# Kernel tuning notes

Measured on AMD Instinct MI355X. Metric: run time of the kernel, lower is better.

The kernel has to match this reference:

```python
import jax, jax.numpy as jnp
import numpy as np

ALPHA = 0.2          # LeakyReLU negative slope
NEG_BIG = -9e15      # zero_vec value used before softmax masking


def setup_inputs() -> dict:
    key = jax.random.key(0)
    k1, k2, k3, k4, k5 = jax.random.split(key, 5)
    N, M, F, K = 2048, 8192, 1024, 10
    feature_matrix = jax.random.normal(k1, (N, F), dtype=jnp.float32)
    embed_matrix = jax.random.normal(k2, (M, F), dtype=jnp.float32)
    # Xavier-ish scaling for params
    weight = jax.random.normal(k3, (F, F), dtype=jnp.float32) * (1.0 / np.sqrt(F))
    a = jax.random.normal(k4, (2 * F, 1), dtype=jnp.float32) * (1.0 / np.sqrt(2 * F))
    neigh_idx = jax.random.randint(k5, (N, K), 0, M, dtype=jnp.int64)
    return {
        "feature_matrix": feature_matrix,
        "embed_matrix": embed_matrix,
        "weight": weight,
        "a": a,
        "neigh_idx": neigh_idx,
    }


def reference(feature_matrix, embed_matrix, weight, a, neigh_idx):
    # feature_matrix: [N, F] features of batch nodes
    # embed_matrix:   [M, F] features of unique sampled neighbors
    # neigh_idx:      [N, K] sampled neighbor columns (set semantics: dups collapse)
    N, F = feature_matrix.shape
    M = embed_matrix.shape[0]
    rows = jnp.arange(N)[:, None]
    mask = jnp.zeros((N, M), dtype=feature_matrix.dtype).at[rows, neigh_idx].set(1.0)

    # GAT kernel path
    hf = feature_matrix @ weight          # [N, F]
    he = embed_matrix @ weight            # [M, F]
    # e_ij = leakyrelu([h_i || h_j] . a) == leakyrelu(h_i.a1 + h_j.a2)
    a1 = a[:F, 0]
    a2 = a[F:, 0]
    e = (hf @ a1)[:, None] + (he @ a2)[None, :]          # [N, M]
    e = jnp.where(e > 0, e, ALPHA * e)                   # LeakyReLU(0.2)
    scores = jnp.where(mask > 0, e, NEG_BIG)
    attention = jax.nn.softmax(scores, axis=1)           # row softmax
    to_feats = attention @ he                            # [N, F]
    return to_feats
```

## Files before the change

### kernel.cpp

```cpp
#include <hip/hip_runtime.h>
#include <math.h>

#define ALPHA 0.2f
#define MAXK 10

typedef _Float16 half8 __attribute__((ext_vector_type(8)));
typedef _Float16 half4 __attribute__((ext_vector_type(4)));
typedef float f32x4 __attribute__((ext_vector_type(4)));

__device__ __forceinline__ void gload_lds16(const void* g, void* l) {
    __builtin_amdgcn_global_load_lds(
        (const __attribute__((address_space(1))) unsigned int*)g,
        (__attribute__((address_space(3))) unsigned int*)l, 16, 0, 0);
}

__global__ void wa_kernel(const float* __restrict__ W, const float* __restrict__ a,
                          float* __restrict__ wa, int F) {
    int wave = (int)((blockIdx.x * blockDim.x + threadIdx.x) >> 6);
    int lane = threadIdx.x & 63;
    if (wave >= F) return;
    const float4* wr = reinterpret_cast<const float4*>(W + (size_t)wave * F);
    const float4* a1 = reinterpret_cast<const float4*>(a);
    const float4* a2 = reinterpret_cast<const float4*>(a + F);
    float acc1 = 0.f, acc2 = 0.f;
    int F4 = F >> 2;
    for (int c = lane; c < F4; c += 64) {
        float4 w = wr[c];
        float4 x = a1[c];
        float4 y = a2[c];
        acc1 += w.x * x.x + w.y * x.y + w.z * x.z + w.w * x.w;
        acc2 += w.x * y.x + w.y * y.y + w.z * y.z + w.w * y.w;
    }
    #pragma unroll
    for (int off = 32; off; off >>= 1) {
        acc1 += __shfl_down(acc1, off);
        acc2 += __shfl_down(acc2, off);
    }
    if (lane == 0) { wa[wave] = acc1; wa[F + wave] = acc2; }
}

__global__ __launch_bounds__(256) void mid_kernel(
    const float* __restrict__ feat, const float* __restrict__ embed,
    const int* __restrict__ nidx, const float* __restrict__ wa,
    const float* __restrict__ W, _Float16* __restrict__ agg,
    _Float16* __restrict__ Wt, int F, int N) {
    const int tid = threadIdx.x;

    if ((int)blockIdx.x >= N) {
        __shared__ float t[32][33];
        const int tb = blockIdx.x - N;
        const int tpr = F >> 5;
        const int bx = (tb % tpr) * 32;
        const int by = (tb / tpr) * 32;
        const int x = tid & 31, y = tid >> 5;
        for (int i = y; i < 32; i += 8)
            t[i][x] = W[(size_t)(bx + i) * F + by + x];
        __syncthreads();
        for (int i = y; i < 32; i += 8)
            Wt[(size_t)(by + i) * F + bx + x] = (_Float16)t[x][i];
        return;
    }

    const int i = blockIdx.x;
    const int f = tid * 4;

    int idx[MAXK];
    bool dup[MAXK];
    #pragma unroll
    for (int k = 0; k < MAXK; k++) idx[k] = nidx[i * MAXK + k];
    #pragma unroll
    for (int k = 0; k < MAXK; k++) {
        bool d = false;
        #pragma unroll
        for (int p = 0; p < MAXK; p++)
            if (p < k) d |= (idx[p] == idx[k]);
        dup[k] = d;
    }

    float4 wa1 = *(const float4*)&wa[f];
    float4 wa2 = *(const float4*)&wa[F + f];
    float4 fv  = *(const float4*)&feat[(size_t)i * F + f];
    float a1p = fv.x * wa1.x + fv.y * wa1.y + fv.z * wa1.z + fv.w * wa1.w;

    float4 rv[MAXK];
    float a2p[MAXK];
    #pragma unroll
    for (int k = 0; k < MAXK; k++) {
        rv[k] = *(const float4*)&embed[(size_t)idx[k] * F + f];
        a2p[k] = rv[k].x * wa2.x + rv[k].y * wa2.y + rv[k].z * wa2.z + rv[k].w * wa2.w;
    }

    #pragma unroll
    for (int off = 32; off; off >>= 1) {
        a1p += __shfl_down(a1p, off);
        #pragma unroll
        for (int k = 0; k < MAXK; k++) a2p[k] += __shfl_down(a2p[k], off);
    }
    __shared__ float red[MAXK + 1][4];
    const int w = tid >> 6, l = tid & 63;
    if (l == 0) {
        red[0][w] = a1p;
        #pragma unroll
        for (int k = 0; k < MAXK; k++) red[k + 1][w] = a2p[k];
    }
    __syncthreads();

    float s1 = red[0][0] + red[0][1] + red[0][2] + red[0][3];
    float sc[MAXK];
    float m = -INFINITY;
    #pragma unroll
    for (int k = 0; k < MAXK; k++) {
        float v = s1 + red[k + 1][0] + red[k + 1][1] + red[k + 1][2] + red[k + 1][3];
        v = v > 0.f ? v : ALPHA * v;
        sc[k] = v;
        if (!dup[k]) m = fmaxf(m, v);
    }
    float sum = 0.f;
    #pragma unroll
    for (int k = 0; k < MAXK; k++) {
        sc[k] = dup[k] ? 0.f : expf(sc[k] - m);
        sum += sc[k];
    }
    float inv = 1.0f / sum;

    float4 o = make_float4(0.f, 0.f, 0.f, 0.f);
    #pragma unroll
    for (int k = 0; k < MAXK; k++) {
        float wk = sc[k] * inv;
        o.x += wk * rv[k].x;
        o.y += wk * rv[k].y;
        o.z += wk * rv[k].z;
        o.w += wk * rv[k].w;
    }
    half4 h = { (_Float16)o.x, (_Float16)o.y, (_Float16)o.z, (_Float16)o.w };
    *(half4*)&agg[(size_t)i * F + f] = h;
}

__global__ __launch_bounds__(256) void gemm_f16_kernel(
    const _Float16* __restrict__ A, const _Float16* __restrict__ Bt,
    float* __restrict__ C, int M, int N, int K) {
    __shared__ _Float16 As[2][64 * 128];
    __shared__ _Float16 Bs[2][64 * 128];
    const int tid = threadIdx.x;

    int bid = blockIdx.y * gridDim.x + blockIdx.x;
    int nwg = gridDim.x * gridDim.y;
    int cpx = nwg >> 3;
    int wg = (bid & 7) * cpx + (bid >> 3);
    const int m0 = (wg / gridDim.x) * 64;
    const int n0 = (wg % gridDim.x) * 64;

    const int l = tid & 63, wv = tid >> 6;
    const int wm = wv >> 1, wn = wv & 1;
    const int lrow = l & 15, kc = l >> 4;
    const int nt = K >> 7;

    f32x4 acc[2][2] = {};

    #define STAGE(bf, t)                                                            \
    do {                                                                            \
        int k0_ = (t) * 128;                                                        \
        _Pragma("unroll")                                                           \
        for (int j_ = 0; j_ < 4; j_++) {                                            \
            int u_ = wv * 256 + j_ * 64 + l;                                        \
            int row_ = u_ >> 4, slot_ = (u_ & 15) ^ (row_ & 7);                     \
            gload_lds16(&A[(size_t)(m0 + row_) * K + k0_ + slot_ * 8],              \
                        (void*)((char*)&As[bf][0] + u_ * 16));                      \
        }                                                                           \
        _Pragma("unroll")                                                           \
        for (int j_ = 0; j_ < 4; j_++) {                                            \
            int u_ = wv * 256 + j_ * 64 + l;                                        \
            int row_ = u_ >> 4, slot_ = (u_ & 15) ^ (row_ & 7);                     \
            gload_lds16(&Bt[(size_t)(n0 + row_) * K + k0_ + slot_ * 8],             \
                        (void*)((char*)&Bs[bf][0] + u_ * 16));                      \
        }                                                                           \
    } while (0)

    STAGE(0, 0);

    int buf = 0;
    for (int t = 0; t < nt; ++t) {
        if (t + 1 < nt) {
            STAGE(buf ^ 1, t + 1);
            asm volatile("s_waitcnt vmcnt(8)" ::: "memory");
        } else {
            asm volatile("s_waitcnt vmcnt(0)" ::: "memory");
        }
        __builtin_amdgcn_s_barrier();
        __builtin_amdgcn_sched_barrier(0);

        __builtin_amdgcn_s_setprio(1);
        #pragma unroll
        for (int ks = 0; ks < 4; ks++) {
            half8 av[2], bv[2];
            #pragma unroll
            for (int fq = 0; fq < 2; fq++) {
                int arow = wm * 32 + fq * 16 + lrow;
                int ag = (ks * 4 + kc) ^ (arow & 7);
                av[fq] = *(const half8*)((const char*)&As[buf][0] + arow * 256 + ag * 16);
                int brow = wn * 32 + fq * 16 + lrow;
                int bg = (ks * 4 + kc) ^ (brow & 7);
                bv[fq] = *(const half8*)((const char*)&Bs[buf][0] + brow * 256 + bg * 16);
            }
            #pragma unroll
            for (int fq = 0; fq < 2; fq++)
                #pragma unroll
                for (int g = 0; g < 2; g++)
                    acc[fq][g] = __builtin_amdgcn_mfma_f32_16x16x32_f16(
                        av[fq], bv[g], acc[fq][g], 0, 0, 0);
        }
        __builtin_amdgcn_s_setprio(0);

        __builtin_amdgcn_sched_barrier(0);
        __builtin_amdgcn_s_barrier();
        buf ^= 1;
    }
    #undef STAGE

    #pragma unroll
    for (int fq = 0; fq < 2; fq++)
        #pragma unroll
        for (int g = 0; g < 2; g++)
            #pragma unroll
            for (int r = 0; r < 4; r++)
                C[(size_t)(m0 + wm * 32 + fq * 16 + kc * 4 + r) * N
                  + n0 + wn * 32 + g * 16 + lrow] = acc[fq][g][r];
}

extern "C" void kernel_launch(void* const* d_in, const int* in_sizes, int n_in,
                              void* d_out, int out_size, void* d_ws, size_t ws_size,
                              hipStream_t stream) {
    const float* feat  = (const float*)d_in[0];
    const float* embed = (const float*)d_in[1];
    const float* W     = (const float*)d_in[2];
    const float* a     = (const float*)d_in[3];
    const int*   nidx  = (const int*)d_in[4];

    int F = in_sizes[3] / 2;
    int N = in_sizes[0] / F;
    int M = in_sizes[1] / F;

    float* ws = (float*)d_ws;
    float* wa = ws;
    _Float16* agg_f16 = (_Float16*)(wa + 2 * F);
    _Float16* wt_f16  = agg_f16 + (size_t)N * F;
    (void)M;

    wa_kernel<<<(F * 64 + 255) / 256, 256, 0, stream>>>(W, a, wa, F);
    {
        int tblocks = (F / 32) * (F / 32);
        mid_kernel<<<N + tblocks, 256, 0, stream>>>(feat, embed, nidx, wa, W,
                                                    agg_f16, wt_f16, F, N);
    }
    {
        dim3 grid(F / 64, N / 64);
        gemm_f16_kernel<<<grid, 256, 0, stream>>>(agg_f16, wt_f16, (float*)d_out, N, F, F);
    }
}
```

Measured before the change: 36.79 us.

## Map one wavefront per row in aggregation kernel to drop block-level reduction

The aggregation part of mid_kernel now processes four rows per 256-thread block, one row per wavefront, instead of one row per block. Each lane covers four float4 chunks of the feature dimension, so the scores are reduced entirely with xor shuffles and the shared-memory reduction plus __syncthreads is gone. In exchange, the gathered embedding rows are no longer held in registers between score and aggregation; they are reloaded from global memory (likely L2-cached) for the weighted sum. The hard-coded 4x64 chunk loop assumes F == 1024 and N divisible by 4.

```diff
diff --git a/kernel.cpp b/kernel.cpp
--- a/kernel.cpp
+++ b/kernel.cpp
@@ -12,6 +12,10 @@
     __builtin_amdgcn_global_load_lds(
         (const __attribute__((address_space(1))) unsigned int*)g,
         (__attribute__((address_space(3))) unsigned int*)l, 16, 0, 0);
+}
+
+__device__ __forceinline__ float dot4(float4 a, float4 b) {
+    return a.x * b.x + a.y * b.y + a.z * b.z + a.w * b.w;
 }
 
 __global__ void wa_kernel(const float* __restrict__ W, const float* __restrict__ a,
@@ -28,8 +32,8 @@
         float4 w = wr[c];
         float4 x = a1[c];
         float4 y = a2[c];
-        acc1 += w.x * x.x + w.y * x.y + w.z * x.z + w.w * x.w;
-        acc2 += w.x * y.x + w.y * y.y + w.z * y.z + w.w * y.w;
+        acc1 += dot4(w, x);
+        acc2 += dot4(w, y);
     }
     #pragma unroll
     for (int off = 32; off; off >>= 1) {
@@ -45,10 +49,11 @@
     const float* __restrict__ W, _Float16* __restrict__ agg,
     _Float16* __restrict__ Wt, int F, int N) {
     const int tid = threadIdx.x;
-
-    if ((int)blockIdx.x >= N) {
+    const int nAgg = N >> 2;
+
+    if ((int)blockIdx.x >= nAgg) {
         __shared__ float t[32][33];
-        const int tb = blockIdx.x - N;
+        const int tb = blockIdx.x - nAgg;
         const int tpr = F >> 5;
         const int bx = (tb % tpr) * 32;
         const int by = (tb / tpr) * 32;
@@ -61,8 +66,13 @@
         return;
     }
 
-    const int i = blockIdx.x;
-    const int f = tid * 4;
+    const int wv = tid >> 6, lane = tid & 63;
+    const int i = (blockIdx.x << 2) | wv;
+    const int F4 = F >> 2;
+
+    const float4* e4 = reinterpret_cast<const float4*>(embed);
+    const float4* f4 = reinterpret_cast<const float4*>(feat);
+    const float4* w4 = reinterpret_cast<const float4*>(wa);
 
     int idx[MAXK];
     bool dup[MAXK];
@@ -77,40 +87,39 @@
         dup[k] = d;
     }
 
-    float4 wa1 = *(const float4*)&wa[f];
-    float4 wa2 = *(const float4*)&wa[F + f];
-    float4 fv  = *(const float4*)&feat[(size_t)i * F + f];
-    float a1p = fv.x * wa1.x + fv.y * wa1.y + fv.z * wa1.z + fv.w * wa1.w;
-
-    float4 rv[MAXK];
+    float4 w2[4];
+    #pragma unroll
+    for (int j = 0; j < 4; j++) w2[j] = w4[F4 + j * 64 + lane];
+
+    float a1p = 0.f;
+    #pragma unroll
+    for (int j = 0; j < 4; j++) {
+        float4 fv = f4[(size_t)i * F4 + j * 64 + lane];
+        float4 w1 = w4[j * 64 + lane];
+        a1p += dot4(fv, w1);
+    }
     float a2p[MAXK];
     #pragma unroll
     for (int k = 0; k < MAXK; k++) {
-        rv[k] = *(const float4*)&embed[(size_t)idx[k] * F + f];
-        a2p[k] = rv[k].x * wa2.x + rv[k].y * wa2.y + rv[k].z * wa2.z + rv[k].w * wa2.w;
+        float s = 0.f;
+        #pragma unroll
+        for (int j = 0; j < 4; j++)
+            s += dot4(e4[(size_t)idx[k] * F4 + j * 64 + lane], w2[j]);
+        a2p[k] = s;
     }
 
     #pragma unroll
     for (int off = 32; off; off >>= 1) {
-        a1p += __shfl_down(a1p, off);
-        #pragma unroll
-        for (int k = 0; k < MAXK; k++) a2p[k] += __shfl_down(a2p[k], off);
-    }
-    __shared__ float red[MAXK + 1][4];
-    const int w = tid >> 6, l = tid & 63;
-    if (l == 0) {
-        red[0][w] = a1p;
-        #pragma unroll
-        for (int k = 0; k < MAXK; k++) red[k + 1][w] = a2p[k];
-    }
-    __syncthreads();
-
-    float s1 = red[0][0] + red[0][1] + red[0][2] + red[0][3];
+        a1p += __shfl_xor(a1p, off);
+        #pragma unroll
+        for (int k = 0; k < MAXK; k++) a2p[k] += __shfl_xor(a2p[k], off);
+    }
+
     float sc[MAXK];
     float m = -INFINITY;
     #pragma unroll
     for (int k = 0; k < MAXK; k++) {
-        float v = s1 + red[k + 1][0] + red[k + 1][1] + red[k + 1][2] + red[k + 1][3];
+        float v = a1p + a2p[k];
         v = v > 0.f ? v : ALPHA * v;
         sc[k] = v;
         if (!dup[k]) m = fmaxf(m, v);
@@ -122,18 +131,24 @@
         sum += sc[k];
     }
     float inv = 1.0f / sum;
-
-    float4 o = make_float4(0.f, 0.f, 0.f, 0.f);
-    #pragma unroll
-    for (int k = 0; k < MAXK; k++) {
-        float wk = sc[k] * inv;
-        o.x += wk * rv[k].x;
-        o.y += wk * rv[k].y;
-        o.z += wk * rv[k].z;
-        o.w += wk * rv[k].w;
-    }
-    half4 h = { (_Float16)o.x, (_Float16)o.y, (_Float16)o.z, (_Float16)o.w };
-    *(half4*)&agg[(size_t)i * F + f] = h;
+    #pragma unroll
+    for (int k = 0; k < MAXK; k++) sc[k] *= inv;
+
+    #pragma unroll
+    for (int j = 0; j < 4; j++) {
+        float4 o = make_float4(0.f, 0.f, 0.f, 0.f);
+        #pragma unroll
+        for (int k = 0; k < MAXK; k++) {
+            float4 rv = e4[(size_t)idx[k] * F4 + j * 64 + lane];
+            float wk = sc[k];
+            o.x += wk * rv.x;
+            o.y += wk * rv.y;
+            o.z += wk * rv.z;
+            o.w += wk * rv.w;
+        }
+        half4 h = { (_Float16)o.x, (_Float16)o.y, (_Float16)o.z, (_Float16)o.w };
+        *(half4*)&agg[(size_t)i * F + j * 256 + lane * 4] = h;
+    }
 }
 
 __global__ __launch_bounds__(256) void gemm_f16_kernel(
@@ -249,8 +264,8 @@
     wa_kernel<<<(F * 64 + 255) / 256, 256, 0, stream>>>(W, a, wa, F);
     {
         int tblocks = (F / 32) * (F / 32);
-        mid_kernel<<<N + tblocks, 256, 0, stream>>>(feat, embed, nidx, wa, W,
-                                                    agg_f16, wt_f16, F, N);
+        mid_kernel<<<N / 4 + tblocks, 256, 0, stream>>>(feat, embed, nidx, wa, W,
+                                                        agg_f16, wt_f16, F, N);
     }
     {
         dim3 grid(F / 64, N / 64);
```

New measurement: 47.03 us. +27.8%, slower.
